# Optimization experiments

Hardware: AMD Instinct MI355X
Metric: run time of the kernel (lower is better)

Reference implementation:

```python
import jax, jax.numpy as jnp
import numpy as np
import math

DIM = 512
BLOCK_NUM = 16
SEQ_LEN = 8192
BLOCK_LEN = SEQ_LEN // BLOCK_NUM  # 512 == DIM -> mask used as-is
BATCH = 4
LN_EPS = 1e-3  # keras LayerNormalization default epsilon


def setup_inputs() -> dict:
    key = jax.random.key(0)
    ks = jax.random.split(key, 5)
    inputs = jax.random.normal(ks[0], (BATCH, BLOCK_NUM, BLOCK_LEN, DIM), dtype=jnp.float32)
    # binary padding-style mask, values in {0,1}
    mask_array = jax.random.randint(ks[1], (BATCH, SEQ_LEN, DIM), 0, 2).astype(jnp.float32)
    scale = 1.0 / math.sqrt(DIM)
    dw1 = jax.random.normal(ks[2], (DIM, DIM), dtype=jnp.float32) * scale
    dw2 = jax.random.normal(ks[3], (DIM, DIM), dtype=jnp.float32) * scale
    dw3 = jax.random.normal(ks[4], (DIM, DIM), dtype=jnp.float32) * scale
    db1 = jnp.zeros((DIM,), dtype=jnp.float32)
    db2 = jnp.zeros((DIM,), dtype=jnp.float32)
    db3 = jnp.zeros((DIM,), dtype=jnp.float32)
    return {"inputs": inputs, "mask_array": mask_array,
            "dw1": dw1, "dw2": dw2, "dw3": dw3,
            "db1": db1, "db2": db2, "db3": db3}


def reference(inputs, mask_array, dw1, dw2, dw3, db1, db2, db3):
    # inputs: [B, block_num, block_len, dim]
    Q = jnp.matmul(inputs, dw1) + db1
    K = jnp.matmul(inputs, dw2) + db2
    V = jnpp_matmul = jnp.matmul(inputs, dw3) + db3
    V = jnp.matmul(inputs, dw3) + db3
    # block-local attention scores: [B, bn, bl, bl]
    scores = jnp.einsum('bnqd,bnkd->bnqk', Q, K) / math.sqrt(DIM)
    # mask: [B, seq_len, dim] -> [B, bn, bl, dim]; block_len == dim so no slice/tile
    m = mask_array.reshape(BATCH, BLOCK_NUM, BLOCK_LEN, DIM)
    scores = scores + (1.0 - m) * jnp.float32(-1e10)
    p = jax.nn.softmax(scores, axis=-1)
    out = jnp.einsum('bnqk,bnkd->bnqd', p, V) + inputs  # residual
    # LayerNorm(axis=-1), fresh keras layer: gamma=1, beta=0, eps=1e-3
    mean = jnp.mean(out, axis=-1, keepdims=True)
    var = jnp.mean(jnp.square(out - mean), axis=-1, keepdims=True)
    return (out - mean) / jnp.sqrt(var + LN_EPS)
```

## Files before the change

### kernel.cpp

```cpp
#include <hip/hip_runtime.h>

#define DIMK 512
#define NBLK 64
#define NTOK 32768

typedef short  short8 __attribute__((ext_vector_type(8)));
typedef float  f32x4  __attribute__((ext_vector_type(4)));
typedef unsigned short u16x8 __attribute__((ext_vector_type(8)));

__device__ __forceinline__ unsigned short f2bf(float f) {
  union { float f; unsigned u; } v; v.f = f;
  unsigned r = (v.u + 0x7FFFu + ((v.u >> 16) & 1u)) >> 16;
  return (unsigned short)r;
}
__device__ __forceinline__ float bf2f(unsigned short h) {
  return __uint_as_float(((unsigned)h) << 16);
}

__device__ __forceinline__ void gload_lds16(const unsigned short* g,
                                            unsigned short* l) {
  __builtin_amdgcn_global_load_lds(
      (const __attribute__((address_space(1))) unsigned int*)(g),
      (__attribute__((address_space(3))) unsigned int*)(l),
      16, 0, 0);
}

__global__ __launch_bounds__(256) void k_wt_prep(
    const float* __restrict__ dw1, const float* __restrict__ dw2,
    const float* __restrict__ dw3, unsigned short* __restrict__ Wt)
{
  __shared__ float t[64][65];
  const int b = blockIdx.x;
  const int w = b >> 6;
  const int tt = b & 63;
  const int kt = (tt >> 3) * 64;
  const int nt = (tt & 7) * 64;
  const float* dw = (w == 0) ? dw1 : (w == 1) ? dw2 : dw3;
  const int tid = threadIdx.x;
  const int rr = tid >> 4;
  const int cc = (tid & 15) << 2;

#pragma unroll
  for (int p = 0; p < 4; ++p) {
    const int r = rr + p * 16;
    const float4 v = *(const float4*)&dw[(size_t)(kt + r) * 512 + nt + cc];
    t[cc + 0][r] = v.x; t[cc + 1][r] = v.y;
    t[cc + 2][r] = v.z; t[cc + 3][r] = v.w;
  }
  __syncthreads();
#pragma unroll
  for (int p = 0; p < 4; ++p) {
    const int r = rr + p * 16;
    ushort4 o;
    o.x = f2bf(t[r][cc + 0]); o.y = f2bf(t[r][cc + 1]);
    o.z = f2bf(t[r][cc + 2]); o.w = f2bf(t[r][cc + 3]);
    *(ushort4*)&Wt[(size_t)w * 262144 + (size_t)(nt + r) * 512 + kt + cc] = o;
  }
}

__global__ __launch_bounds__(256) void k_xconv(
    const float* __restrict__ X, unsigned short* __restrict__ Xb)
{
  const size_t i = ((size_t)blockIdx.x * 256 + threadIdx.x) * 8;
  const float4 a = *(const float4*)(X + i);
  const float4 b = *(const float4*)(X + i + 4);
  u16x8 o;
  o[0] = f2bf(a.x); o[1] = f2bf(a.y); o[2] = f2bf(a.z); o[3] = f2bf(a.w);
  o[4] = f2bf(b.x); o[5] = f2bf(b.y); o[6] = f2bf(b.z); o[7] = f2bf(b.w);
  *(u16x8*)(Xb + i) = o;
}

__global__ __launch_bounds__(256) void k_bitpack(
    const float* __restrict__ mask, unsigned char* __restrict__ bits)
{
  const size_t gid = (size_t)blockIdx.x * 256 + threadIdx.x;
  const size_t i = gid * 8;
  const float4 ma = *(const float4*)(mask + i);
  const float4 mb = *(const float4*)(mask + i + 4);
  unsigned v = 0;
  v |= (ma.x > 0.5f) << 0; v |= (ma.y > 0.5f) << 1;
  v |= (ma.z > 0.5f) << 2; v |= (ma.w > 0.5f) << 3;
  v |= (mb.x > 0.5f) << 4; v |= (mb.y > 0.5f) << 5;
  v |= (mb.z > 0.5f) << 6; v |= (mb.w > 0.5f) << 7;
  bits[gid] = (unsigned char)v;
}

__global__ __launch_bounds__(256, 2) void k_qkv(
    const unsigned short* __restrict__ Xb, const unsigned short* __restrict__ Wt,
    const float* __restrict__ db1, const float* __restrict__ db2,
    const float* __restrict__ db3,
    unsigned short* __restrict__ Qb, unsigned short* __restrict__ Kb,
    unsigned short* __restrict__ Vt)
{
  __shared__ __align__(16) unsigned short smem[32768];

  const int id = blockIdx.x;
  const int x = id & 7, j = id >> 3;
  const int mtile = x * 32 + (j >> 2);
  const int nt = j & 3;
  const size_t m0 = (size_t)mtile * 128;
  const int n0 = nt * 128;

  const int tid = threadIdx.x, lane = tid & 63, wv = tid >> 6;
  const int quad = lane >> 4, l16 = lane & 15;
  const int rb = (wv >> 1) * 64, cb = (wv & 1) * 64;

  f32x4 acc[3][4][4];
#pragma unroll
  for (int w = 0; w < 3; ++w)
#pragma unroll
    for (int i = 0; i < 4; ++i)
#pragma unroll
      for (int jj = 0; jj < 4; ++jj) {
        f32x4 z = {0.f, 0.f, 0.f, 0.f}; acc[w][i][jj] = z;
      }

  const int ra0 = tid >> 2,          oa0 = (tid & 3) << 3;
  const int ra1 = (tid + 256) >> 2,  oa1 = ((tid + 256) & 3) << 3;
  const unsigned short* a0 = &Xb[(m0 + ra0) * (size_t)DIMK + oa0];
  const unsigned short* a1 = &Xb[(m0 + ra1) * (size_t)DIMK + oa1];

  auto stage = [&](unsigned short* base, int it) {
    const int k0 = it * 32;
    gload_lds16(a0 + k0, base + tid * 8);
    gload_lds16(a1 + k0, base + (tid + 256) * 8);
#pragma unroll
    for (int h = 0; h < 6; ++h) {
      const int c = tid + h * 256;
      const int w = c >> 9, cc = c & 511;
      const int r = cc >> 2, o = (cc & 3) << 3;
      gload_lds16(&Wt[(size_t)w * 262144 + (size_t)(n0 + r) * 512 + k0 + o],
                  base + 4096 + w * 4096 + cc * 8);
    }
  };

  stage(smem, 0);
  __syncthreads();
  int cur = 0;
  for (int it = 0; it < 16; ++it) {
    unsigned short* cbuf = smem + cur * 16384;
    if (it < 15) stage(smem + (cur ^ 1) * 16384, it + 1);
    const unsigned short* As = cbuf;
    const unsigned short* Bs = cbuf + 4096;
    short8 af[4];
#pragma unroll
    for (int i = 0; i < 4; ++i)
      af[i] = *(const short8*)&As[(rb + i * 16 + l16) * 32 + quad * 8];
#pragma unroll
    for (int jj = 0; jj < 4; ++jj)
#pragma unroll
      for (int w = 0; w < 3; ++w) {
        const short8 bf =
            *(const short8*)&Bs[w * 4096 + (cb + jj * 16 + l16) * 32 + quad * 8];
#pragma unroll
        for (int i = 0; i < 4; ++i)
          acc[w][i][jj] = __builtin_amdgcn_mfma_f32_16x16x32_bf16(
              af[i], bf, acc[w][i][jj], 0, 0, 0);
      }
    __syncthreads();
    cur ^= 1;
  }

#pragma unroll
  for (int w = 0; w < 2; ++w) {
    const float* db = (w == 0) ? db1 : db2;
    unsigned short* Ob = (w == 0) ? Qb : Kb;
#pragma unroll
    for (int i = 0; i < 4; ++i)
#pragma unroll
      for (int jj = 0; jj < 4; ++jj)
#pragma unroll
        for (int r = 0; r < 4; ++r) {
          const size_t row = m0 + rb + i * 16 + quad * 4 + r;
          const int col = n0 + cb + jj * 16 + l16;
          Ob[row * (size_t)DIMK + col] = f2bf(acc[w][i][jj][r] + db[col]);
        }
  }
#pragma unroll
  for (int i = 0; i < 4; ++i)
#pragma unroll
    for (int jj = 0; jj < 4; ++jj) {
      const int cl = cb + jj * 16 + l16;
      const int t0 = rb + i * 16 + quad * 4;
      const float bv = db3[n0 + cl];
      ushort4 pk;
      pk.x = f2bf(acc[2][i][jj][0] + bv);
      pk.y = f2bf(acc[2][i][jj][1] + bv);
      pk.z = f2bf(acc[2][i][jj][2] + bv);
      pk.w = f2bf(acc[2][i][jj][3] + bv);
      *(ushort4*)&smem[cl * 136 + t0] = pk;
    }
  __syncthreads();
  const int blk = mtile >> 2;
  const int tokbase = (mtile & 3) * 128;
  unsigned short* Vblk = Vt + (size_t)blk * 262144;
#pragma unroll
  for (int h = 0; h < 8; ++h) {
    const int c = tid + h * 256;
    const int cl = c >> 4, toff = (c & 15) * 8;
    *(u16x8*)&Vblk[(size_t)(n0 + cl) * 512 + tokbase + toff] =
        *(const u16x8*)&smem[cl * 136 + toff];
  }
}

__global__ __launch_bounds__(256, 2) void k_attn_p(
    const unsigned short* __restrict__ Qb, const unsigned short* __restrict__ Kb,
    const unsigned long long* __restrict__ bits, unsigned short* __restrict__ Pb)
{
  __shared__ __align__(16) unsigned short smem[36864];
  __shared__ float red[4][64];
  const int tid = threadIdx.x, lane = tid & 63, wv = tid >> 6;
  const int quad = lane >> 4, l16 = lane & 15;
  const int blk = blockIdx.x & 63, mt = blockIdx.x >> 6;
  const size_t tb = (size_t)blk * 512;
  const size_t q0 = tb + (size_t)mt * 64;

  f32x4 acc[4][8];
#pragma unroll
  for (int i = 0; i < 4; ++i)
#pragma unroll
    for (int j = 0; j < 8; ++j) { f32x4 z = {0.f, 0.f, 0.f, 0.f}; acc[i][j] = z; }

  const int ra = tid >> 2, oa = (tid & 3) << 3;
  const unsigned short* ap = &Qb[(q0 + ra) * (size_t)DIMK + oa];
  const unsigned short* kp = &Kb[tb * (size_t)DIMK];

  auto stage = [&](unsigned short* base, int it) {
    const int k0 = it * 32;
    gload_lds16(ap + k0, base + tid * 8);
#pragma unroll
    for (int h = 0; h < 8; ++h) {
      const int c = tid + h * 256;
      const int r = c >> 2, o = (c & 3) << 3;
      gload_lds16(kp + (size_t)r * DIMK + k0 + o, base + 2048 + c * 8);
    }
  };

  stage(smem, 0);
  __syncthreads();
  int cur = 0;
  for (int it = 0; it < 16; ++it) {
    unsigned short* cbuf = smem + cur * 18432;
    if (it < 15) stage(smem + (cur ^ 1) * 18432, it + 1);
    const unsigned short* As = cbuf;
    const unsigned short* Bs = cbuf + 2048;
    short8 af[4], bfv[8];
#pragma unroll
    for (int i = 0; i < 4; ++i)
      af[i] = *(const short8*)&As[(i * 16 + l16) * 32 + quad * 8];
#pragma unroll
    for (int j = 0; j < 8; ++j)
      bfv[j] = *(const short8*)&Bs[(wv * 128 + j * 16 + l16) * 32 + quad * 8];
#pragma unroll
    for (int i = 0; i < 4; ++i)
#pragma unroll
      for (int j = 0; j < 8; ++j)
        acc[i][j] = __builtin_amdgcn_mfma_f32_16x16x32_bf16(
            af[i], bfv[j], acc[i][j], 0, 0, 0);
    __syncthreads();
    cur ^= 1;
  }

  const float scale = 0.04419417382415922f;
  float rmax[4][4];
#pragma unroll
  for (int i = 0; i < 4; ++i)
#pragma unroll
    for (int r = 0; r < 4; ++r) rmax[i][r] = -3.0e38f;
#pragma unroll
  for (int i = 0; i < 4; ++i)
#pragma unroll
    for (int r = 0; r < 4; ++r) {
      const size_t tok = q0 + i * 16 + quad * 4 + r;
      const unsigned long long w0 = bits[tok * 8 + wv * 2];
      const unsigned long long w1 = bits[tok * 8 + wv * 2 + 1];
#pragma unroll
      for (int j = 0; j < 8; ++j) {
        const unsigned long long sel = (j < 4) ? w0 : w1;
        const float bias = ((sel >> (l16 + 16 * (j & 3))) & 1ull) ? 0.0f : -1e10f;
        const float v = acc[i][j][r] * scale + bias;
        acc[i][j][r] = v;
        rmax[i][r] = fmaxf(rmax[i][r], v);
      }
    }
#pragma unroll
  for (int i = 0; i < 4; ++i)
#pragma unroll
    for (int r = 0; r < 4; ++r)
      for (int d = 1; d < 16; d <<= 1)
        rmax[i][r] = fmaxf(rmax[i][r], __shfl_xor(rmax[i][r], d, 64));
  if (l16 == 0)
#pragma unroll
    for (int i = 0; i < 4; ++i)
#pragma unroll
      for (int r = 0; r < 4; ++r) red[wv][i * 16 + quad * 4 + r] = rmax[i][r];
  __syncthreads();
#pragma unroll
  for (int i = 0; i < 4; ++i)
#pragma unroll
    for (int r = 0; r < 4; ++r) {
      const int row = i * 16 + quad * 4 + r;
      rmax[i][r] = fmaxf(fmaxf(red[0][row], red[1][row]),
                         fmaxf(red[2][row], red[3][row]));
    }
  __syncthreads();
  float rsum[4][4];
#pragma unroll
  for (int i = 0; i < 4; ++i)
#pragma unroll
    for (int r = 0; r < 4; ++r) rsum[i][r] = 0.f;
#pragma unroll
  for (int i = 0; i < 4; ++i)
#pragma unroll
    for (int j = 0; j < 8; ++j)
#pragma unroll
      for (int r = 0; r < 4; ++r) {
        const float e = __expf(acc[i][j][r] - rmax[i][r]);
        acc[i][j][r] = e;
        rsum[i][r] += e;
      }
#pragma unroll
  for (int i = 0; i < 4; ++i)
#pragma unroll
    for (int r = 0; r < 4; ++r)
      for (int d = 1; d < 16; d <<= 1)
        rsum[i][r] += __shfl_xor(rsum[i][r], d, 64);
  if (l16 == 0)
#pragma unroll
    for (int i = 0; i < 4; ++i)
#pragma unroll
      for (int r = 0; r < 4; ++r) red[wv][i * 16 + quad * 4 + r] = rsum[i][r];
  __syncthreads();
#pragma unroll
  for (int i = 0; i < 4; ++i)
#pragma unroll
    for (int r = 0; r < 4; ++r) {
      const int row = i * 16 + quad * 4 + r;
      rsum[i][r] = 1.0f / (red[0][row] + red[1][row] + red[2][row] + red[3][row]);
    }
#pragma unroll
  for (int i = 0; i < 4; ++i)
#pragma unroll
    for (int j = 0; j < 8; ++j)
#pragma unroll
      for (int r = 0; r < 4; ++r) {
        const size_t tok = q0 + i * 16 + quad * 4 + r;
        const int col = wv * 128 + j * 16 + l16;
        Pb[tok * (size_t)DIMK + col] = f2bf(acc[i][j][r] * rsum[i][r]);
      }
}

__global__ __launch_bounds__(256, 2) void k_pv_ln(
    const unsigned short* __restrict__ Pb, const unsigned short* __restrict__ Vt,
    const unsigned short* __restrict__ Xb, float* __restrict__ Out)
{
  __shared__ __align__(16) unsigned short smem[36864];
  __shared__ float2 red[4][64];
  const int tid = threadIdx.x, lane = tid & 63, wv = tid >> 6;
  const int quad = lane >> 4, l16 = lane & 15;
  const int blk = blockIdx.x & 63, mt = blockIdx.x >> 6;
  const size_t tb = (size_t)blk * 512;
  const size_t q0 = tb + (size_t)mt * 64;

  f32x4 acc[4][8];
#pragma unroll
  for (int i = 0; i < 4; ++i)
#pragma unroll
    for (int j = 0; j < 8; ++j) { f32x4 z = {0.f, 0.f, 0.f, 0.f}; acc[i][j] = z; }

  const int ra = tid >> 2, oa = (tid & 3) << 3;
  const unsigned short* ap = &Pb[(q0 + ra) * (size_t)DIMK + oa];
  const unsigned short* vp = Vt + (size_t)blk * 262144;

  auto stage = [&](unsigned short* base, int it) {
    const int k0 = it * 32;
    gload_lds16(ap + k0, base + tid * 8);
#pragma unroll
    for (int h = 0; h < 8; ++h) {
      const int c = tid + h * 256;
      const int r = c >> 2, o = (c & 3) << 3;
      gload_lds16(vp + (size_t)r * DIMK + k0 + o, base + 2048 + c * 8);
    }
  };

  stage(smem, 0);
  __syncthreads();
  int cur = 0;
  for (int it = 0; it < 16; ++it) {
    unsigned short* cbuf = smem + cur * 18432;
    if (it < 15) stage(smem + (cur ^ 1) * 18432, it + 1);
    const unsigned short* As = cbuf;
    const unsigned short* Bs = cbuf + 2048;
    short8 af[4], bfv[8];
#pragma unroll
    for (int i = 0; i < 4; ++i)
      af[i] = *(const short8*)&As[(i * 16 + l16) * 32 + quad * 8];
#pragma unroll
    for (int j = 0; j < 8; ++j)
      bfv[j] = *(const short8*)&Bs[(wv * 128 + j * 16 + l16) * 32 + quad * 8];
#pragma unroll
    for (int i = 0; i < 4; ++i)
#pragma unroll
      for (int j = 0; j < 8; ++j)
        acc[i][j] = __builtin_amdgcn_mfma_f32_16x16x32_bf16(
            af[i], bfv[j], acc[i][j], 0, 0, 0);
    __syncthreads();
    cur ^= 1;
  }

  float vsum[4][4], vsq[4][4];
#pragma unroll
  for (int i = 0; i < 4; ++i)
#pragma unroll
    for (int r = 0; r < 4; ++r) { vsum[i][r] = 0.f; vsq[i][r] = 0.f; }
#pragma unroll
  for (int i = 0; i < 4; ++i)
#pragma unroll
    for (int j = 0; j < 8; ++j)
#pragma unroll
      for (int r = 0; r < 4; ++r) {
        const size_t tok = q0 + i * 16 + quad * 4 + r;
        const int col = wv * 128 + j * 16 + l16;
        const float v = acc[i][j][r] + bf2f(Xb[tok * (size_t)DIMK + col]);
        acc[i][j][r] = v;
        vsum[i][r] += v;
        vsq[i][r] += v * v;
      }
#pragma unroll
  for (int i = 0; i < 4; ++i)
#pragma unroll
    for (int r = 0; r < 4; ++r)
      for (int d = 1; d < 16; d <<= 1) {
        vsum[i][r] += __shfl_xor(vsum[i][r], d, 64);
        vsq[i][r]  += __shfl_xor(vsq[i][r], d, 64);
      }
  if (l16 == 0)
#pragma unroll
    for (int i = 0; i < 4; ++i)
#pragma unroll
      for (int r = 0; r < 4; ++r) {
        float2 p; p.x = vsum[i][r]; p.y = vsq[i][r];
        red[wv][i * 16 + quad * 4 + r] = p;
      }
  __syncthreads();
#pragma unroll
  for (int i = 0; i < 4; ++i)
#pragma unroll
    for (int r = 0; r < 4; ++r) {
      const int row = i * 16 + quad * 4 + r;
      float s = 0.f, q = 0.f;
#pragma unroll
      for (int w = 0; w < 4; ++w) { s += red[w][row].x; q += red[w][row].y; }
      const float mean = s * (1.0f / 512.0f);
      const float var  = q * (1.0f / 512.0f) - mean * mean;
      vsum[i][r] = mean;
      vsq[i][r]  = rsqrtf(var + 1e-3f);
    }
#pragma unroll
  for (int i = 0; i < 4; ++i)
#pragma unroll
    for (int j = 0; j < 8; ++j)
#pragma unroll
      for (int r = 0; r < 4; ++r) {
        const size_t tok = q0 + i * 16 + quad * 4 + r;
        const int col = wv * 128 + j * 16 + l16;
        Out[tok * (size_t)DIMK + col] =
            (acc[i][j][r] - vsum[i][r]) * vsq[i][r];
      }
}

extern "C" void kernel_launch(void* const* d_in, const int* in_sizes, int n_in,
                              void* d_out, int out_size, void* d_ws, size_t ws_size,
                              hipStream_t stream)
{
  const float* X    = (const float*)d_in[0];
  const float* mask = (const float*)d_in[1];
  const float* dw1  = (const float*)d_in[2];
  const float* dw2  = (const float*)d_in[3];
  const float* dw3  = (const float*)d_in[4];
  const float* db1  = (const float*)d_in[5];
  const float* db2  = (const float*)d_in[6];
  const float* db3  = (const float*)d_in[7];
  float* Out = (float*)d_out;

  char* ws = (char*)d_ws;
  const size_t MB = 1ull << 20;
  unsigned short* Wt = (unsigned short*)(ws);
  unsigned short* Qb = (unsigned short*)(ws + 2 * MB);
  unsigned short* Kb = (unsigned short*)(ws + 34 * MB);
  unsigned short* Vt = (unsigned short*)(ws + 66 * MB);
  unsigned short* Xb = (unsigned short*)(ws + 98 * MB);
  unsigned short* Pb = Qb;
  unsigned char*  bits = (unsigned char*)d_out;

  k_wt_prep<<<192, 256, 0, stream>>>(dw1, dw2, dw3, Wt);
  k_xconv  <<<8192, 256, 0, stream>>>(X, Xb);
  k_bitpack<<<8192, 256, 0, stream>>>(mask, bits);
  k_qkv    <<<1024, 256, 0, stream>>>(Xb, Wt, db1, db2, db3, Qb, Kb, Vt);
  k_attn_p <<<512, 256, 0, stream>>>(Qb, Kb, (const unsigned long long*)bits, Pb);
  k_pv_ln  <<<512, 256, 0, stream>>>(Pb, Vt, Xb, Out);
}
```

Before: 326.6 us.

## Store intermediate bf16 tensors in k-slab tiled layout for contiguous LDS staging

All intermediate bf16 buffers (Xb, Wt, Q, K, Vt, P) are rewritten in a blocked layout where each 32-wide k-slab for a tile is contiguous. Global-to-LDS staging loads in the GEMM kernels then read one contiguous chunk per iteration instead of many strided 64-byte row pieces. This is meant to improve DRAM/L2 access efficiency and simplify address computation. The cost is scattered scalar stores in the epilogues (Q, K, P, and residual Xb reads), which may be less coalesced.

```diff
diff --git a/kernel.cpp b/kernel.cpp
--- a/kernel.cpp
+++ b/kernel.cpp
@@ -24,6 +24,7 @@
       (__attribute__((address_space(3))) unsigned int*)(l),
       16, 0, 0);
 }
+
 
 __global__ __launch_bounds__(256) void k_wt_prep(
     const float* __restrict__ dw1, const float* __restrict__ dw2,
@@ -51,23 +52,30 @@
 #pragma unroll
   for (int p = 0; p < 4; ++p) {
     const int r = rr + p * 16;
+    const int n = nt + r;
+    const int k = kt + cc;
     ushort4 o;
     o.x = f2bf(t[r][cc + 0]); o.y = f2bf(t[r][cc + 1]);
     o.z = f2bf(t[r][cc + 2]); o.w = f2bf(t[r][cc + 3]);
-    *(ushort4*)&Wt[(size_t)w * 262144 + (size_t)(nt + r) * 512 + kt + cc] = o;
+    *(ushort4*)&Wt[(size_t)w * 262144 + (size_t)(k >> 5) * 16384 +
+                   (size_t)n * 32 + (k & 31)] = o;
   }
 }
 
 __global__ __launch_bounds__(256) void k_xconv(
     const float* __restrict__ X, unsigned short* __restrict__ Xb)
 {
-  const size_t i = ((size_t)blockIdx.x * 256 + threadIdx.x) * 8;
+  const size_t gid = (size_t)blockIdx.x * 256 + threadIdx.x;
+  const size_t i = gid * 8;
+  const int tok = (int)(i >> 9);
+  const int col = (int)(i & 511);
   const float4 a = *(const float4*)(X + i);
   const float4 b = *(const float4*)(X + i + 4);
   u16x8 o;
   o[0] = f2bf(a.x); o[1] = f2bf(a.y); o[2] = f2bf(a.z); o[3] = f2bf(a.w);
   o[4] = f2bf(b.x); o[5] = f2bf(b.y); o[6] = f2bf(b.z); o[7] = f2bf(b.w);
-  *(u16x8*)(Xb + i) = o;
+  *(u16x8*)(Xb + ((size_t)(tok >> 7) * 16 + (col >> 5)) * 4096 +
+            (tok & 127) * 32 + (col & 31)) = o;
 }
 
 __global__ __launch_bounds__(256) void k_bitpack(
@@ -98,7 +106,7 @@
   const int x = id & 7, j = id >> 3;
   const int mtile = x * 32 + (j >> 2);
   const int nt = j & 3;
-  const size_t m0 = (size_t)mtile * 128;
+  const int m0 = mtile * 128;
   const int n0 = nt * 128;
 
   const int tid = threadIdx.x, lane = tid & 63, wv = tid >> 6;
@@ -115,22 +123,17 @@
         f32x4 z = {0.f, 0.f, 0.f, 0.f}; acc[w][i][jj] = z;
       }
 
-  const int ra0 = tid >> 2,          oa0 = (tid & 3) << 3;
-  const int ra1 = (tid + 256) >> 2,  oa1 = ((tid + 256) & 3) << 3;
-  const unsigned short* a0 = &Xb[(m0 + ra0) * (size_t)DIMK + oa0];
-  const unsigned short* a1 = &Xb[(m0 + ra1) * (size_t)DIMK + oa1];
-
   auto stage = [&](unsigned short* base, int it) {
-    const int k0 = it * 32;
-    gload_lds16(a0 + k0, base + tid * 8);
-    gload_lds16(a1 + k0, base + (tid + 256) * 8);
+    const unsigned short* aslab = Xb + ((size_t)mtile * 16 + it) * 4096;
+    gload_lds16(aslab + tid * 8, base + tid * 8);
+    gload_lds16(aslab + (tid + 256) * 8, base + (tid + 256) * 8);
 #pragma unroll
     for (int h = 0; h < 6; ++h) {
       const int c = tid + h * 256;
       const int w = c >> 9, cc = c & 511;
-      const int r = cc >> 2, o = (cc & 3) << 3;
-      gload_lds16(&Wt[(size_t)w * 262144 + (size_t)(n0 + r) * 512 + k0 + o],
-                  base + 4096 + w * 4096 + cc * 8);
+      const unsigned short* bslab =
+          Wt + (size_t)w * 262144 + (size_t)it * 16384 + (size_t)n0 * 32;
+      gload_lds16(bslab + cc * 8, base + 4096 + w * 4096 + cc * 8);
     }
   };
 
@@ -162,20 +165,18 @@
   }
 
 #pragma unroll
-  for (int w = 0; w < 2; ++w) {
-    const float* db = (w == 0) ? db1 : db2;
-    unsigned short* Ob = (w == 0) ? Qb : Kb;
-#pragma unroll
-    for (int i = 0; i < 4; ++i)
-#pragma unroll
-      for (int jj = 0; jj < 4; ++jj)
-#pragma unroll
-        for (int r = 0; r < 4; ++r) {
-          const size_t row = m0 + rb + i * 16 + quad * 4 + r;
-          const int col = n0 + cb + jj * 16 + l16;
-          Ob[row * (size_t)DIMK + col] = f2bf(acc[w][i][jj][r] + db[col]);
-        }
-  }
+  for (int i = 0; i < 4; ++i)
+#pragma unroll
+    for (int jj = 0; jj < 4; ++jj)
+#pragma unroll
+      for (int r = 0; r < 4; ++r) {
+        const int tok = m0 + rb + i * 16 + quad * 4 + r;
+        const int col = n0 + cb + jj * 16 + l16;
+        Qb[((size_t)(tok >> 6) * 16 + (col >> 5)) * 2048 +
+           (tok & 63) * 32 + (col & 31)] = f2bf(acc[0][i][jj][r] + db1[col]);
+        Kb[((size_t)(tok >> 9) * 16 + (col >> 5)) * 16384 +
+           (tok & 511) * 32 + (col & 31)] = f2bf(acc[1][i][jj][r] + db2[col]);
+      }
 #pragma unroll
   for (int i = 0; i < 4; ++i)
 #pragma unroll
@@ -191,15 +192,13 @@
       *(ushort4*)&smem[cl * 136 + t0] = pk;
     }
   __syncthreads();
-  const int blk = mtile >> 2;
-  const int tokbase = (mtile & 3) * 128;
-  unsigned short* Vblk = Vt + (size_t)blk * 262144;
 #pragma unroll
   for (int h = 0; h < 8; ++h) {
     const int c = tid + h * 256;
     const int cl = c >> 4, toff = (c & 15) * 8;
-    *(u16x8*)&Vblk[(size_t)(n0 + cl) * 512 + tokbase + toff] =
-        *(const u16x8*)&smem[cl * 136 + toff];
+    const int tg = mtile * 128 + toff;
+    *(u16x8*)&Vt[(size_t)(tg >> 5) * 16384 + (size_t)(n0 + cl) * 32 +
+                 (tg & 31)] = *(const u16x8*)&smem[cl * 136 + toff];
   }
 }
 
@@ -212,8 +211,8 @@
   const int tid = threadIdx.x, lane = tid & 63, wv = tid >> 6;
   const int quad = lane >> 4, l16 = lane & 15;
   const int blk = blockIdx.x & 63, mt = blockIdx.x >> 6;
-  const size_t tb = (size_t)blk * 512;
-  const size_t q0 = tb + (size_t)mt * 64;
+  const size_t q0 = (size_t)blk * 512 + (size_t)mt * 64;
+  const int qt = blk * 8 + mt;
 
   f32x4 acc[4][8];
 #pragma unroll
@@ -221,18 +220,14 @@
 #pragma unroll
     for (int j = 0; j < 8; ++j) { f32x4 z = {0.f, 0.f, 0.f, 0.f}; acc[i][j] = z; }
 
-  const int ra = tid >> 2, oa = (tid & 3) << 3;
-  const unsigned short* ap = &Qb[(q0 + ra) * (size_t)DIMK + oa];
-  const unsigned short* kp = &Kb[tb * (size_t)DIMK];
-
   auto stage = [&](unsigned short* base, int it) {
-    const int k0 = it * 32;
-    gload_lds16(ap + k0, base + tid * 8);
+    const unsigned short* aslab = Qb + ((size_t)qt * 16 + it) * 2048;
+    gload_lds16(aslab + tid * 8, base + tid * 8);
+    const unsigned short* bslab = Kb + ((size_t)blk * 16 + it) * 16384;
 #pragma unroll
     for (int h = 0; h < 8; ++h) {
       const int c = tid + h * 256;
-      const int r = c >> 2, o = (c & 3) << 3;
-      gload_lds16(kp + (size_t)r * DIMK + k0 + o, base + 2048 + c * 8);
+      gload_lds16(bslab + c * 8, base + 2048 + c * 8);
     }
   };
 
@@ -344,9 +339,10 @@
     for (int j = 0; j < 8; ++j)
 #pragma unroll
       for (int r = 0; r < 4; ++r) {
-        const size_t tok = q0 + i * 16 + quad * 4 + r;
+        const int tok = (int)(q0 + i * 16 + quad * 4 + r);
         const int col = wv * 128 + j * 16 + l16;
-        Pb[tok * (size_t)DIMK + col] = f2bf(acc[i][j][r] * rsum[i][r]);
+        Pb[((size_t)(tok >> 6) * 16 + (col >> 5)) * 2048 +
+           (tok & 63) * 32 + (col & 31)] = f2bf(acc[i][j][r] * rsum[i][r]);
       }
 }
 
@@ -359,8 +355,8 @@
   const int tid = threadIdx.x, lane = tid & 63, wv = tid >> 6;
   const int quad = lane >> 4, l16 = lane & 15;
   const int blk = blockIdx.x & 63, mt = blockIdx.x >> 6;
-  const size_t tb = (size_t)blk * 512;
-  const size_t q0 = tb + (size_t)mt * 64;
+  const size_t q0 = (size_t)blk * 512 + (size_t)mt * 64;
+  const int qt = blk * 8 + mt;
 
   f32x4 acc[4][8];
 #pragma unroll
@@ -368,18 +364,14 @@
 #pragma unroll
     for (int j = 0; j < 8; ++j) { f32x4 z = {0.f, 0.f, 0.f, 0.f}; acc[i][j] = z; }
 
-  const int ra = tid >> 2, oa = (tid & 3) << 3;
-  const unsigned short* ap = &Pb[(q0 + ra) * (size_t)DIMK + oa];
-  const unsigned short* vp = Vt + (size_t)blk * 262144;
-
   auto stage = [&](unsigned short* base, int it) {
-    const int k0 = it * 32;
-    gload_lds16(ap + k0, base + tid * 8);
+    const unsigned short* aslab = Pb + ((size_t)qt * 16 + it) * 2048;
+    gload_lds16(aslab + tid * 8, base + tid * 8);
+    const unsigned short* bslab = Vt + ((size_t)blk * 16 + it) * 16384;
 #pragma unroll
     for (int h = 0; h < 8; ++h) {
       const int c = tid + h * 256;
-      const int r = c >> 2, o = (c & 3) << 3;
-      gload_lds16(vp + (size_t)r * DIMK + k0 + o, base + 2048 + c * 8);
+      gload_lds16(bslab + c * 8, base + 2048 + c * 8);
     }
   };
 
@@ -419,9 +411,11 @@
     for (int j = 0; j < 8; ++j)
 #pragma unroll
       for (int r = 0; r < 4; ++r) {
-        const size_t tok = q0 + i * 16 + quad * 4 + r;
+        const int tok = (int)(q0 + i * 16 + quad * 4 + r);
         const int col = wv * 128 + j * 16 + l16;
-        const float v = acc[i][j][r] + bf2f(Xb[tok * (size_t)DIMK + col]);
+        const float v = acc[i][j][r] +
+            bf2f(Xb[((size_t)(tok >> 7) * 16 + (col >> 5)) * 4096 +
+                    (tok & 127) * 32 + (col & 31)]);
         acc[i][j][r] = v;
         vsum[i][r] += v;
         vsq[i][r] += v * v;
```

New measurement: 302.8 us. 7.3% less time.
